# Kernel tuning notes

Hardware: AMD Instinct MI355X
Metric: run time of the kernel (lower is better)

The kernel has to match this reference:

```python
import jax, jax.numpy as jnp
import numpy as np

N = 50000      # nodes
E = 800000     # edges (avg degree 16)
D_IN = 128
H = 128
D_OUT = 32


def setup_inputs() -> dict:
    key = jax.random.key(0)
    ks = jax.random.split(key, 12)
    s = 0.05
    return {
        "x": jax.random.normal(ks[0], (N, D_IN), jnp.float32),
        "edge_index": jax.random.randint(ks[1], (2, E), 0, N, jnp.int32),
        "W_in": jax.random.normal(ks[2], (D_IN, H), jnp.float32) * s,
        "b_in": jnp.zeros((H,), jnp.float32),
        "W_msg0": jax.random.normal(ks[3], (H, H), jnp.float32) * s,
        "gru_wih0": jax.random.normal(ks[4], (3 * H, H), jnp.float32) * s,
        "gru_whh0": jax.random.normal(ks[5], (3 * H, H), jnp.float32) * s,
        "gru_bih0": jnp.zeros((3 * H,), jnp.float32),
        "gru_bhh0": jnp.zeros((3 * H,), jnp.float32),
        "W_msg1": jax.random.normal(ks[6], (H, H), jnp.float32) * s,
        "gru_wih1": jax.random.normal(ks[7], (3 * H, H), jnp.float32) * s,
        "gru_whh1": jax.random.normal(ks[8], (3 * H, H), jnp.float32) * s,
        "gru_bih1": jnp.zeros((3 * H,), jnp.float32),
        "gru_bhh1": jnp.zeros((3 * H,), jnp.float32),
        "W_out": jax.random.normal(ks[9], (H, D_OUT), jnp.float32) * s,
        "b_out": jnp.zeros((D_OUT,), jnp.float32),
    }


def _gated_layer(h, src, dst, W_msg, wih, whh, bih, bhh):
    # GatedGraphConv (num_layers=1): linear -> scatter-add over edges -> GRU update
    m = h @ W_msg                                           # [N, H]
    agg = jax.ops.segment_sum(m[src], dst, num_segments=N)  # gather at src, add at dst
    gi = agg @ wih.T + bih                                  # [N, 3H]
    gh = h @ whh.T + bhh                                    # [N, 3H]
    i_r, i_z, i_n = jnp.split(gi, 3, axis=-1)
    h_r, h_z, h_n = jnp.split(gh, 3, axis=-1)
    r = jax.nn.sigmoid(i_r + h_r)
    z = jax.nn.sigmoid(i_z + h_z)
    n = jnp.tanh(i_n + r * h_n)
    return (1.0 - z) * n + z * h


def reference(x, edge_index, W_in, b_in,
              W_msg0, gru_wih0, gru_whh0, gru_bih0, gru_bhh0,
              W_msg1, gru_wih1, gru_whh1, gru_bih1, gru_bhh1,
              W_out, b_out):
    src, dst = edge_index[0], edge_index[1]
    h = jax.nn.relu(x @ W_in + b_in)
    h = _gated_layer(h, src, dst, W_msg0, gru_wih0, gru_whh0, gru_bih0, gru_bhh0)
    h = _gated_layer(h, src, dst, W_msg1, gru_wih1, gru_whh1, gru_bih1, gru_bhh1)
    return h @ W_out + b_out
```

## Files before the change

### kernel.cpp

```cpp
#include <hip/hip_runtime.h>
#include <hip/hip_bf16.h>
#include <math.h>

#define NN 50000
#define NE 800000
#define HD 128
#define SCAN_BLOCKS 196
#define FILL_CHUNK 4096
#define FILL_CHUNKS ((NE + FILL_CHUNK - 1) / FILL_CHUNK)
#define NPART 8
#define HIST_BLOCKS ((NE + 255) / 256)

typedef __attribute__((ext_vector_type(8))) short bf16x8;
typedef __attribute__((ext_vector_type(4))) float f32x4;

__device__ inline float b2f(unsigned short s) {
    union { unsigned int u; float f; } w; w.u = ((unsigned int)s) << 16; return w.f;
}
__device__ inline short f2b(float f) {
    __hip_bfloat16 h = __float2bfloat16(f);
    short s; __builtin_memcpy(&s, &h, 2); return s;
}

__global__ void prep_kernel(const int* __restrict__ dst, int* __restrict__ counts,
                            const float* W_in, const float* W_msg0, const float* W_msg1,
                            const float* W_out, const float* wih0, const float* whh0,
                            const float* wih1, const float* whh1,
                            short* pWin, short* pWm0, short* pWm1, short* pWout,
                            short* pI0, short* pH0, short* pI1, short* pH1) {
    int b = blockIdx.x;
    if (b < HIST_BLOCKS) {
        int e = b * 256 + threadIdx.x;
        if (e < NE) atomicAdd(&counts[dst[e]], 1);
        return;
    }
    int pb = b - HIST_BLOCKS;
    int px = pb % 24, wsel = pb / 24;
    const float* src; short* dstp; int JT; bool kmajor; int J;
    switch (wsel) {
        case 0: src = W_in;   dstp = pWin;  JT = 8;  kmajor = true;  J = 128; break;
        case 1: src = W_msg0; dstp = pWm0;  JT = 8;  kmajor = true;  J = 128; break;
        case 2: src = W_msg1; dstp = pWm1;  JT = 8;  kmajor = true;  J = 128; break;
        case 3: src = W_out;  dstp = pWout; JT = 2;  kmajor = true;  J = 32;  break;
        case 4: src = wih0;   dstp = pI0;   JT = 24; kmajor = false; J = 384; break;
        case 5: src = whh0;   dstp = pH0;   JT = 24; kmajor = false; J = 384; break;
        case 6: src = wih1;   dstp = pI1;   JT = 24; kmajor = false; J = 384; break;
        default: src = whh1;  dstp = pH1;   JT = 24; kmajor = false; J = 384; break;
    }
    int t = px * 256 + threadIdx.x;
    if (t >= JT * 4 * 64) return;
    int l = t & 63, ks = (t >> 6) & 3, jt = t >> 8;
    int j = jt * 16 + (l & 15);
    int k0 = ks * 32 + (l >> 4) * 8;
    bf16x8 tv;
    if (kmajor) {
        #pragma unroll
        for (int i = 0; i < 8; ++i) tv[i] = f2b(src[(k0 + i) * J + j]);
    } else {
        #pragma unroll
        for (int i = 0; i < 8; ++i) tv[i] = f2b(src[j * 128 + k0 + i]);
    }
    *reinterpret_cast<bf16x8*>(dstp + t * 8) = tv;
}

__global__ __launch_bounds__(256) void scan_partial_kernel(const int* __restrict__ counts,
                                                           int* __restrict__ partial) {
    __shared__ int sm[256];
    int i = blockIdx.x * 256 + threadIdx.x;
    sm[threadIdx.x] = (i < NN) ? counts[i] : 0;
    __syncthreads();
    for (int off = 128; off > 0; off >>= 1) {
        if (threadIdx.x < off) sm[threadIdx.x] += sm[threadIdx.x + off];
        __syncthreads();
    }
    if (threadIdx.x == 0) partial[blockIdx.x] = sm[0];
}

__global__ __launch_bounds__(256) void scan_base_kernel(const int* __restrict__ partial,
                                                        int* __restrict__ base) {
    __shared__ int sm[256];
    int tid = threadIdx.x;
    int v = (tid < SCAN_BLOCKS) ? partial[tid] : 0;
    sm[tid] = v;
    __syncthreads();
    for (int off = 1; off < 256; off <<= 1) {
        int t = (tid >= off) ? sm[tid - off] : 0;
        __syncthreads();
        sm[tid] += t;
        __syncthreads();
    }
    if (tid < SCAN_BLOCKS) base[tid] = sm[tid] - v;
}

__global__ __launch_bounds__(256) void scan_final_kernel(const int* __restrict__ counts,
                                                         const int* __restrict__ base,
                                                         int* __restrict__ offsets,
                                                         int* __restrict__ cursor) {
    __shared__ int sm[256];
    int tid = threadIdx.x;
    int i = blockIdx.x * 256 + tid;
    int v = (i < NN) ? counts[i] : 0;
    sm[tid] = v;
    __syncthreads();
    for (int off = 1; off < 256; off <<= 1) {
        int t = (tid >= off) ? sm[tid - off] : 0;
        __syncthreads();
        sm[tid] += t;
        __syncthreads();
    }
    if (i < NN) {
        int o = base[blockIdx.x] + sm[tid] - v;
        offsets[i] = o;
        cursor[i]  = o;
        if (i == NN - 1) offsets[NN] = o + v;
    }
}

__global__ __launch_bounds__(256) void fill_part_kernel(const int* __restrict__ src,
                                                        const int* __restrict__ dst,
                                                        int* __restrict__ cursor,
                                                        int* __restrict__ perm_src) {
    int part  = blockIdx.x & (NPART - 1);
    int chunk = blockIdx.x >> 3;
    int lo = part * (NN / NPART);
    int hi = (part == NPART - 1) ? NN : lo + (NN / NPART);
    int e0 = chunk * FILL_CHUNK;
    int e1 = min(e0 + FILL_CHUNK, NE);
    for (int e = e0 + threadIdx.x; e < e1; e += 256) {
        int d = dst[e];
        if (d >= lo && d < hi) {
            int pos = atomicAdd(&cursor[d], 1);
            perm_src[pos] = src[e];
        }
    }
}

__global__ __launch_bounds__(256) void aggregate_bf16(const short* __restrict__ m,
                                                      const int* __restrict__ offsets,
                                                      const int* __restrict__ perm_src,
                                                      short* __restrict__ agg) {
    int node = blockIdx.x * 8 + (threadIdx.x >> 5);
    if (node >= NN) return;
    int q = (threadIdx.x & 31) * 4;
    int beg = offsets[node], end = offsets[node + 1];
    float a0 = 0.f, a1 = 0.f, a2 = 0.f, a3 = 0.f;
    int e = beg;
    for (; e + 2 <= end; e += 2) {
        int s0 = perm_src[e], s1 = perm_src[e + 1];
        ushort4 u0 = *reinterpret_cast<const ushort4*>(m + (size_t)s0 * HD + q);
        ushort4 u1 = *reinterpret_cast<const ushort4*>(m + (size_t)s1 * HD + q);
        a0 += b2f(u0.x) + b2f(u1.x);
        a1 += b2f(u0.y) + b2f(u1.y);
        a2 += b2f(u0.z) + b2f(u1.z);
        a3 += b2f(u0.w) + b2f(u1.w);
    }
    if (e < end) {
        ushort4 u = *reinterpret_cast<const ushort4*>(m + (size_t)perm_src[e] * HD + q);
        a0 += b2f(u.x); a1 += b2f(u.y); a2 += b2f(u.z); a3 += b2f(u.w);
    }
    ushort4 o;
    o.x = (unsigned short)f2b(a0); o.y = (unsigned short)f2b(a1);
    o.z = (unsigned short)f2b(a2); o.w = (unsigned short)f2b(a3);
    *reinterpret_cast<ushort4*>(agg + (size_t)node * HD + q) = o;
}

template<int JT2, bool OUTF32_2>
__device__ inline void second_gemm(const short* hw, int l, int r0,
                                   const short* __restrict__ Bp2,
                                   const float* __restrict__ bias2,
                                   void* __restrict__ Cv2) {
    int lr = l & 15;
    bf16x8 a2[4];
    #pragma unroll
    for (int ks = 0; ks < 4; ++ks) {
        int row = l & 15;
        int col = (ks * 32 + (l >> 4) * 8) ^ ((row & 7) << 3);
        a2[ks] = *reinterpret_cast<const bf16x8*>(hw + row * 128 + col);
    }
    const f32x4 zero = {0.f, 0.f, 0.f, 0.f};
    #pragma unroll
    for (int jt = 0; jt < JT2; ++jt) {
        f32x4 acc = zero;
        const short* bp = Bp2 + ((jt * 4) * 64 + l) * 8;
        #pragma unroll
        for (int ks = 0; ks < 4; ++ks) {
            bf16x8 b = *reinterpret_cast<const bf16x8*>(bp + ks * 64 * 8);
            acc = __builtin_amdgcn_mfma_f32_16x16x32_bf16(a2[ks], b, acc, 0, 0, 0);
        }
        int col = jt * 16 + lr;
        float bs = bias2 ? bias2[col] : 0.f;
        #pragma unroll
        for (int rg = 0; rg < 4; ++rg) {
            int row = r0 + (l >> 4) * 4 + rg;
            if (row < NN) {
                float v = acc[rg] + bs;
                if (OUTF32_2) ((float*)Cv2)[(size_t)row * (16 * JT2) + col] = v;
                else          ((short*)Cv2)[(size_t)row * (16 * JT2) + col] = f2b(v);
            }
        }
    }
}

__global__ __launch_bounds__(256) void fused_in_msg(const float* __restrict__ x,
                                                    const short* __restrict__ Bp1,
                                                    const float* __restrict__ bias1,
                                                    const short* __restrict__ Bp2,
                                                    short* __restrict__ Hout,
                                                    short* __restrict__ Mout) {
    __shared__ short hl[4][2048];
    int w = threadIdx.x >> 6, l = threadIdx.x & 63;
    int r0 = blockIdx.x * 64 + w * 16;
    int lr = l & 15, lk = (l >> 4) * 8;
    short* hw = hl[w];

    bf16x8 a[4];
    {
        int row = min(r0 + lr, NN - 1);
        #pragma unroll
        for (int ks = 0; ks < 4; ++ks) {
            const float* ap = x + (size_t)row * HD + ks * 32 + lk;
            float4 v0 = *(const float4*)ap;
            float4 v1 = *(const float4*)(ap + 4);
            bf16x8 tv;
            tv[0] = f2b(v0.x); tv[1] = f2b(v0.y); tv[2] = f2b(v0.z); tv[3] = f2b(v0.w);
            tv[4] = f2b(v1.x); tv[5] = f2b(v1.y); tv[6] = f2b(v1.z); tv[7] = f2b(v1.w);
            a[ks] = tv;
        }
    }

    const f32x4 zero = {0.f, 0.f, 0.f, 0.f};
    #pragma unroll
    for (int jt = 0; jt < 8; ++jt) {
        f32x4 acc = zero;
        const short* bp = Bp1 + ((jt * 4) * 64 + l) * 8;
        #pragma unroll
        for (int ks = 0; ks < 4; ++ks) {
            bf16x8 b = *reinterpret_cast<const bf16x8*>(bp + ks * 64 * 8);
            acc = __builtin_amdgcn_mfma_f32_16x16x32_bf16(a[ks], b, acc, 0, 0, 0);
        }
        int col = jt * 16 + lr;
        float bs = bias1[col];
        #pragma unroll
        for (int rg = 0; rg < 4; ++rg) {
            int row16 = (l >> 4) * 4 + rg;
            int grow = r0 + row16;
            float v = fmaxf(acc[rg] + bs, 0.f);
            short hb = f2b(v);
            hw[row16 * 128 + (col ^ ((row16 & 7) << 3))] = hb;
            if (grow < NN) Hout[(size_t)grow * HD + col] = hb;
        }
    }
    __syncthreads();
    second_gemm<8, false>(hw, l, r0, Bp2, nullptr, Mout);
}

template<int JT2, bool OUTF32_2, bool WRITE_H>
__global__ __launch_bounds__(256) void fused_gru(const short* __restrict__ agg,
                                                 const short* __restrict__ h,
                                                 const short* __restrict__ BpI,
                                                 const short* __restrict__ BpH,
                                                 const float* __restrict__ bih,
                                                 const float* __restrict__ bhh,
                                                 const short* __restrict__ Bp2,
                                                 const float* __restrict__ bias2,
                                                 short* __restrict__ Hout,
                                                 void* __restrict__ Cv2) {
    __shared__ short hl[4][2048];
    __shared__ short bw[24 * 512];
    int w = threadIdx.x >> 6, l = threadIdx.x & 63;
    int r0 = blockIdx.x * 64 + w * 16;
    int lr = l & 15, lk = (l >> 4) * 8;
    short* hw = hl[w];

    bf16x8 aa[4], ah[4];
    {
        int row = min(r0 + lr, NN - 1);
        #pragma unroll
        for (int ks = 0; ks < 4; ++ks) {
            aa[ks] = *reinterpret_cast<const bf16x8*>(agg + (size_t)row * HD + ks * 32 + lk);
            ah[ks] = *reinterpret_cast<const bf16x8*>(h   + (size_t)row * HD + ks * 32 + lk);
        }
    }

    bf16x8 streg[6];
    auto stage_regs = [&](int jt) {
        #pragma unroll
        for (int i = 0; i < 6; ++i) {
            int c = w + 4 * i;
            int s = c / 12, rem = c % 12, g = rem >> 2, ks = rem & 3;
            const short* p = (s ? BpH : BpI) + g * (8 * 4 * 64 * 8) + ((jt * 4 + ks) * 64 + l) * 8;
            streg[i] = *reinterpret_cast<const bf16x8*>(p);
        }
    };
    auto write_lds = [&]() {
        #pragma unroll
        for (int i = 0; i < 6; ++i) {
            int c = w + 4 * i;
            *reinterpret_cast<bf16x8*>(&bw[c * 512 + l * 8]) = streg[i];
        }
    };

    stage_regs(0);
    const f32x4 zero = {0.f, 0.f, 0.f, 0.f};
    #pragma unroll 1
    for (int jt = 0; jt < 8; ++jt) {
        __syncthreads();
        write_lds();
        if (jt < 7) stage_regs(jt + 1);
        __syncthreads();

        f32x4 ir = zero, iz = zero, in_ = zero;
        f32x4 hr = zero, hz = zero, hn = zero;
        #pragma unroll
        for (int ks = 0; ks < 4; ++ks) {
            bf16x8 bir = *reinterpret_cast<const bf16x8*>(&bw[(0 * 12 + 0 * 4 + ks) * 512 + l * 8]);
            bf16x8 biz = *reinterpret_cast<const bf16x8*>(&bw[(0 * 12 + 1 * 4 + ks) * 512 + l * 8]);
            bf16x8 bin = *reinterpret_cast<const bf16x8*>(&bw[(0 * 12 + 2 * 4 + ks) * 512 + l * 8]);
            bf16x8 bhr = *reinterpret_cast<const bf16x8*>(&bw[(1 * 12 + 0 * 4 + ks) * 512 + l * 8]);
            bf16x8 bhz = *reinterpret_cast<const bf16x8*>(&bw[(1 * 12 + 1 * 4 + ks) * 512 + l * 8]);
            bf16x8 bhn = *reinterpret_cast<const bf16x8*>(&bw[(1 * 12 + 2 * 4 + ks) * 512 + l * 8]);
            ir  = __builtin_amdgcn_mfma_f32_16x16x32_bf16(aa[ks], bir, ir,  0, 0, 0);
            iz  = __builtin_amdgcn_mfma_f32_16x16x32_bf16(aa[ks], biz, iz,  0, 0, 0);
            in_ = __builtin_amdgcn_mfma_f32_16x16x32_bf16(aa[ks], bin, in_, 0, 0, 0);
            hr  = __builtin_amdgcn_mfma_f32_16x16x32_bf16(ah[ks], bhr, hr,  0, 0, 0);
            hz  = __builtin_amdgcn_mfma_f32_16x16x32_bf16(ah[ks], bhz, hz,  0, 0, 0);
            hn  = __builtin_amdgcn_mfma_f32_16x16x32_bf16(ah[ks], bhn, hn,  0, 0, 0);
        }
        int col = jt * 16 + lr;
        float bir_ = bih[col], biz_ = bih[128 + col], bin_ = bih[256 + col];
        float bhr_ = bhh[col], bhz_ = bhh[128 + col], bhn_ = bhh[256 + col];
        #pragma unroll
        for (int rg = 0; rg < 4; ++rg) {
            int row16 = (l >> 4) * 4 + rg;
            int grow = r0 + row16;
            int crow = min(grow, NN - 1);
            float rr = 1.f / (1.f + __expf(-(ir[rg] + bir_ + hr[rg] + bhr_)));
            float zz = 1.f / (1.f + __expf(-(iz[rg] + biz_ + hz[rg] + bhz_)));
            float pre = in_[rg] + bin_ + rr * (hn[rg] + bhn_);
            pre = fminf(fmaxf(pre, -20.f), 20.f);
            float e2 = __expf(2.f * pre);
            float nn_ = (e2 - 1.f) / (e2 + 1.f);
            float hv = b2f((unsigned short)h[(size_t)crow * HD + col]);
            float nh = (1.f - zz) * nn_ + zz * hv;
            short hb = f2b(nh);
            hw[row16 * 128 + (col ^ ((row16 & 7) << 3))] = hb;
            if (WRITE_H && grow < NN) Hout[(size_t)grow * HD + col] = hb;
        }
    }
    __syncthreads();
    second_gemm<JT2, OUTF32_2>(hw, l, r0, Bp2, bias2, Cv2);
}

extern "C" void kernel_launch(void* const* d_in, const int* in_sizes, int n_in,
                              void* d_out, int out_size, void* d_ws, size_t ws_size,
                              hipStream_t stream) {
    const float* x      = (const float*)d_in[0];
    const int*   eidx   = (const int*)d_in[1];
    const float* W_in   = (const float*)d_in[2];
    const float* b_in   = (const float*)d_in[3];
    const float* W_msg0 = (const float*)d_in[4];
    const float* wih0   = (const float*)d_in[5];
    const float* whh0   = (const float*)d_in[6];
    const float* bih0   = (const float*)d_in[7];
    const float* bhh0   = (const float*)d_in[8];
    const float* W_msg1 = (const float*)d_in[9];
    const float* wih1   = (const float*)d_in[10];
    const float* whh1   = (const float*)d_in[11];
    const float* bih1   = (const float*)d_in[12];
    const float* bhh1   = (const float*)d_in[13];
    const float* W_out  = (const float*)d_in[14];
    const float* b_out  = (const float*)d_in[15];
    float* out = (float*)d_out;

    const int* src = eidx;
    const int* dst = eidx + NE;

    char* ws = (char*)d_ws;
    size_t off = 0;
    auto alloc = [&](size_t bytes) {
        void* p = ws + off;
        off += (bytes + 255) & ~(size_t)255;
        return p;
    };
    short* bufA = (short*)alloc((size_t)NN * HD * 2);
    short* bufB = (short*)alloc((size_t)NN * HD * 2);
    short* bufC = (short*)alloc((size_t)NN * HD * 2);
    short* pWin  = (short*)alloc(8  * 4 * 64 * 8 * 2);
    short* pWm0  = (short*)alloc(8  * 4 * 64 * 8 * 2);
    short* pWm1  = (short*)alloc(8  * 4 * 64 * 8 * 2);
    short* pWout = (short*)alloc(2  * 4 * 64 * 8 * 2);
    short* pI0   = (short*)alloc(24 * 4 * 64 * 8 * 2);
    short* pH0   = (short*)alloc(24 * 4 * 64 * 8 * 2);
    short* pI1   = (short*)alloc(24 * 4 * 64 * 8 * 2);
    short* pH1   = (short*)alloc(24 * 4 * 64 * 8 * 2);
    int* counts  = (int*)alloc(NN * 4);
    int* offsets = (int*)alloc((NN + 1) * 4);
    int* cursor  = (int*)alloc(NN * 4);
    int* perm    = (int*)alloc(NE * 4);
    int* partial = (int*)alloc(SCAN_BLOCKS * 4);
    int* pbase   = (int*)alloc(SCAN_BLOCKS * 4);

    hipMemsetAsync(counts, 0, NN * 4, stream);
    prep_kernel<<<HIST_BLOCKS + 192, 256, 0, stream>>>(dst, counts,
        W_in, W_msg0, W_msg1, W_out, wih0, whh0, wih1, whh1,
        pWin, pWm0, pWm1, pWout, pI0, pH0, pI1, pH1);
    scan_partial_kernel<<<SCAN_BLOCKS, 256, 0, stream>>>(counts, partial);
    scan_base_kernel<<<1, 256, 0, stream>>>(partial, pbase);
    scan_final_kernel<<<SCAN_BLOCKS, 256, 0, stream>>>(counts, pbase, offsets, cursor);
    fill_part_kernel<<<NPART * FILL_CHUNKS, 256, 0, stream>>>(src, dst, cursor, perm);

    int g64 = (NN + 63) / 64;

    fused_in_msg<<<g64, 256, 0, stream>>>(x, pWin, b_in, pWm0, bufA, bufB);

    aggregate_bf16<<<(NN + 7) / 8, 256, 0, stream>>>(bufB, offsets, perm, bufC);
    fused_gru<8, false, true><<<g64, 256, 0, stream>>>(bufC, bufA, pI0, pH0, bih0, bhh0,
                                                       pWm1, nullptr, bufB, bufA);

    aggregate_bf16<<<(NN + 7) / 8, 256, 0, stream>>>(bufA, offsets, perm, bufC);
    fused_gru<2, true, false><<<g64, 256, 0, stream>>>(bufC, bufB, pI1, pH1, bih1, bhh1,
                                                       pWout, b_out, nullptr, out);
}
```

Before: 341.8 us.

## Double-buffer GRU weight tiles in LDS and read old h from LDS

Gives the fused_gru weight staging buffer two LDS slots, so the next tile is written after compute and each loop iteration needs one barrier instead of two. The wave's h rows are also stored into its LDS tile up front, so the old h value in the gate blend is read from LDS rather than from scattered global loads. LDS use per block doubles for the weight buffer, which may lower occupancy.

```diff
diff --git a/kernel.cpp b/kernel.cpp
--- a/kernel.cpp
+++ b/kernel.cpp
@@ -266,7 +266,7 @@
                                                  short* __restrict__ Hout,
                                                  void* __restrict__ Cv2) {
     __shared__ short hl[4][2048];
-    __shared__ short bw[24 * 512];
+    __shared__ short bw[2][12288];
     int w = threadIdx.x >> 6, l = threadIdx.x & 63;
     int r0 = blockIdx.x * 64 + w * 16;
     int lr = l & 15, lk = (l >> 4) * 8;
@@ -280,6 +280,11 @@
             aa[ks] = *reinterpret_cast<const bf16x8*>(agg + (size_t)row * HD + ks * 32 + lk);
             ah[ks] = *reinterpret_cast<const bf16x8*>(h   + (size_t)row * HD + ks * 32 + lk);
         }
+    }
+    #pragma unroll
+    for (int ks = 0; ks < 4; ++ks) {
+        int col = ks * 32 + lk;
+        *reinterpret_cast<bf16x8*>(&hw[lr * 128 + (col ^ ((lr & 7) << 3))]) = ah[ks];
     }
 
     bf16x8 streg[6];
@@ -292,33 +297,34 @@
             streg[i] = *reinterpret_cast<const bf16x8*>(p);
         }
     };
-    auto write_lds = [&]() {
+    auto write_lds = [&](int buf) {
         #pragma unroll
         for (int i = 0; i < 6; ++i) {
             int c = w + 4 * i;
-            *reinterpret_cast<bf16x8*>(&bw[c * 512 + l * 8]) = streg[i];
+            *reinterpret_cast<bf16x8*>(&bw[buf][c * 512 + l * 8]) = streg[i];
         }
     };
 
     stage_regs(0);
+    write_lds(0);
+    __syncthreads();
+
     const f32x4 zero = {0.f, 0.f, 0.f, 0.f};
     #pragma unroll 1
     for (int jt = 0; jt < 8; ++jt) {
-        __syncthreads();
-        write_lds();
         if (jt < 7) stage_regs(jt + 1);
-        __syncthreads();
+        const short* bb = bw[jt & 1];
 
         f32x4 ir = zero, iz = zero, in_ = zero;
         f32x4 hr = zero, hz = zero, hn = zero;
         #pragma unroll
         for (int ks = 0; ks < 4; ++ks) {
-            bf16x8 bir = *reinterpret_cast<const bf16x8*>(&bw[(0 * 12 + 0 * 4 + ks) * 512 + l * 8]);
-            bf16x8 biz = *reinterpret_cast<const bf16x8*>(&bw[(0 * 12 + 1 * 4 + ks) * 512 + l * 8]);
-            bf16x8 bin = *reinterpret_cast<const bf16x8*>(&bw[(0 * 12 + 2 * 4 + ks) * 512 + l * 8]);
-            bf16x8 bhr = *reinterpret_cast<const bf16x8*>(&bw[(1 * 12 + 0 * 4 + ks) * 512 + l * 8]);
-            bf16x8 bhz = *reinterpret_cast<const bf16x8*>(&bw[(1 * 12 + 1 * 4 + ks) * 512 + l * 8]);
-            bf16x8 bhn = *reinterpret_cast<const bf16x8*>(&bw[(1 * 12 + 2 * 4 + ks) * 512 + l * 8]);
+            bf16x8 bir = *reinterpret_cast<const bf16x8*>(&bb[(0 * 12 + 0 * 4 + ks) * 512 + l * 8]);
+            bf16x8 biz = *reinterpret_cast<const bf16x8*>(&bb[(0 * 12 + 1 * 4 + ks) * 512 + l * 8]);
+            bf16x8 bin = *reinterpret_cast<const bf16x8*>(&bb[(0 * 12 + 2 * 4 + ks) * 512 + l * 8]);
+            bf16x8 bhr = *reinterpret_cast<const bf16x8*>(&bb[(1 * 12 + 0 * 4 + ks) * 512 + l * 8]);
+            bf16x8 bhz = *reinterpret_cast<const bf16x8*>(&bb[(1 * 12 + 1 * 4 + ks) * 512 + l * 8]);
+            bf16x8 bhn = *reinterpret_cast<const bf16x8*>(&bb[(1 * 12 + 2 * 4 + ks) * 512 + l * 8]);
             ir  = __builtin_amdgcn_mfma_f32_16x16x32_bf16(aa[ks], bir, ir,  0, 0, 0);
             iz  = __builtin_amdgcn_mfma_f32_16x16x32_bf16(aa[ks], biz, iz,  0, 0, 0);
             in_ = __builtin_amdgcn_mfma_f32_16x16x32_bf16(aa[ks], bin, in_, 0, 0, 0);
@@ -333,21 +339,23 @@
         for (int rg = 0; rg < 4; ++rg) {
             int row16 = (l >> 4) * 4 + rg;
             int grow = r0 + row16;
-            int crow = min(grow, NN - 1);
+            int lidx = row16 * 128 + (col ^ ((row16 & 7) << 3));
             float rr = 1.f / (1.f + __expf(-(ir[rg] + bir_ + hr[rg] + bhr_)));
             float zz = 1.f / (1.f + __expf(-(iz[rg] + biz_ + hz[rg] + bhz_)));
             float pre = in_[rg] + bin_ + rr * (hn[rg] + bhn_);
             pre = fminf(fmaxf(pre, -20.f), 20.f);
             float e2 = __expf(2.f * pre);
             float nn_ = (e2 - 1.f) / (e2 + 1.f);
-            float hv = b2f((unsigned short)h[(size_t)crow * HD + col]);
+            float hv = b2f((unsigned short)hw[lidx]);
             float nh = (1.f - zz) * nn_ + zz * hv;
             short hb = f2b(nh);
-            hw[row16 * 128 + (col ^ ((row16 & 7) << 3))] = hb;
+            hw[lidx] = hb;
             if (WRITE_H && grow < NN) Hout[(size_t)grow * HD + col] = hb;
         }
-    }
-    __syncthreads();
+
+        if (jt < 7) write_lds((jt + 1) & 1);
+        __syncthreads();
+    }
     second_gemm<JT2, OUTF32_2>(hw, l, r0, Bp2, bias2, Cv2);
 }
 
```

Result: slower. 350.5 us (+2.5%).
